# Kernel optimization log

Measured on AMD Instinct MI355X. Metric: run time of the kernel, lower is better.

The kernel has to match this reference:

```python
import jax, jax.numpy as jnp
import numpy as np

D_MODEL = 1024
N_HEADS = 16
HEAD_DIM = D_MODEL // N_HEADS
D_FF = 4 * D_MODEL


def _layernorm(x, g, b, eps=1e-5):
    mu = jnp.mean(x, axis=-1, keepdims=True)
    var = jnp.var(x, axis=-1, keepdims=True)
    return (x - mu) * jax.lax.rsqrt(var + eps) * g + b


def setup_inputs() -> dict:
    key = jax.random.key(0)
    ks = jax.random.split(key, 12)
    s = lambda fan_in: 1.0 / np.sqrt(fan_in)
    x = jax.random.normal(ks[0], (2, 2048, D_MODEL), dtype=jnp.float32)
    return {
        "x": x,
        "ln1_g": jnp.ones((D_MODEL,), jnp.float32),
        "ln1_b": jnp.zeros((D_MODEL,), jnp.float32),
        "w_qkv": jax.random.uniform(ks[1], (D_MODEL, 3 * D_MODEL), jnp.float32, -s(D_MODEL), s(D_MODEL)),
        "b_qkv": jax.random.uniform(ks[2], (3 * D_MODEL,), jnp.float32, -s(D_MODEL), s(D_MODEL)),
        "w_out": jax.random.uniform(ks[3], (D_MODEL, D_MODEL), jnp.float32, -s(D_MODEL), s(D_MODEL)),
        "b_out": jax.random.uniform(ks[4], (D_MODEL,), jnp.float32, -s(D_MODEL), s(D_MODEL)),
        "ln2_g": jnp.ones((D_MODEL,), jnp.float32),
        "ln2_b": jnp.zeros((D_MODEL,), jnp.float32),
        "w_ff1": jax.random.uniform(ks[5], (D_MODEL, D_FF), jnp.float32, -s(D_MODEL), s(D_MODEL)),
        "b_ff1": jax.random.uniform(ks[6], (D_FF,), jnp.float32, -s(D_MODEL), s(D_MODEL)),
        "w_ff2": jax.random.uniform(ks[7], (D_FF, D_MODEL), jnp.float32, -s(D_FF), s(D_FF)),
        "b_ff2": jax.random.uniform(ks[8], (D_MODEL,), jnp.float32, -s(D_FF), s(D_FF)),
    }


def reference(x, ln1_g, ln1_b, w_qkv, b_qkv, w_out, b_out,
              ln2_g, ln2_b, w_ff1, b_ff1, w_ff2, b_ff2):
    B, T, C = x.shape
    # --- pre-LN causal self-attention + residual ---
    h = _layernorm(x, ln1_g, ln1_b)
    qkv = h @ w_qkv + b_qkv                                  # [B,T,3C]
    qkv = qkv.reshape(B, T, 3, N_HEADS, HEAD_DIM)
    q, k, v = qkv[:, :, 0], qkv[:, :, 1], qkv[:, :, 2]       # [B,T,H,Dh]
    scores = jnp.einsum("bthd,bshd->bhts", q, k) / np.sqrt(HEAD_DIM).astype(np.float32)
    causal = jnp.tril(jnp.ones((T, T), dtype=bool))
    scores = jnp.where(causal, scores, -jnp.inf)
    weights = jax.nn.softmax(scores, axis=-1)                # [B,H,T,T]
    attn = jnp.einsum("bhts,bshd->bthd", weights, v).reshape(B, T, C)
    x = x + attn @ w_out + b_out
    # --- pre-LN GELU FFN + residual ---
    h = _layernorm(x, ln2_g, ln2_b)
    h = jax.nn.gelu(h @ w_ff1 + b_ff1, approximate=False)    # torch GELU = erf
    x = x + h @ w_ff2 + b_ff2
    return x
```

## Files before the change

kernel.cpp:

```cpp
#include <hip/hip_runtime.h>
#include <hip/hip_bf16.h>
#include <math.h>

#define TSEQ 2048
#define BATCH 2
#define CDIM 1024
#define NH 16
#define HD 64
#define DFF 4096
#define ROWS (BATCH*TSEQ)

typedef __attribute__((ext_vector_type(4))) float f32x4;
typedef __attribute__((ext_vector_type(8))) short bf16x8;
typedef __attribute__((ext_vector_type(4))) unsigned short u16x4;

__device__ __forceinline__ void gload_lds16(const void* g, void* l) {
    void* gv = const_cast<void*>(g);
    __builtin_amdgcn_global_load_lds((__attribute__((address_space(1))) void*)gv,
                                     (__attribute__((address_space(3))) void*)l, 16, 0, 0);
}

__device__ __forceinline__ unsigned short f2bf(float f) {
    unsigned int u = __float_as_uint(f);
    return (unsigned short)((u + 0x7FFFu + ((u >> 16) & 1u)) >> 16);
}
__device__ __forceinline__ float bf2f(unsigned short u) {
    return __uint_as_float((unsigned int)u << 16);
}
__device__ __forceinline__ unsigned int cvt_pk_bf16(float lo, float hi) {
    unsigned int r;
    asm("v_cvt_pk_bf16_f32 %0, %1, %2" : "=v"(r) : "v"(lo), "v"(hi));
    return r;
}
__device__ __forceinline__ float fast_gelu(float v) {
    float u = fmaf(0.044715f * v * v, v, v);
    float e = __expf(-1.5957691216057308f * u);
    return v * __builtin_amdgcn_rcpf(1.0f + e);
}

__global__ __launch_bounds__(256) void ln_kernel(const float* __restrict__ x,
                                                 const float* __restrict__ g,
                                                 const float* __restrict__ b,
                                                 unsigned short* __restrict__ out) {
    int row = blockIdx.x;
    int tid = threadIdx.x;
    const float* xr = x + (size_t)row * CDIM;
    float4 v = *(const float4*)(xr + tid * 4);
    float s  = v.x + v.y + v.z + v.w;
    float s2 = v.x*v.x + v.y*v.y + v.z*v.z + v.w*v.w;
    #pragma unroll
    for (int off = 32; off >= 1; off >>= 1) {
        s  += __shfl_down(s, off);
        s2 += __shfl_down(s2, off);
    }
    __shared__ float red[8];
    int wid = tid >> 6, lane = tid & 63;
    if (lane == 0) { red[wid] = s; red[wid + 4] = s2; }
    __syncthreads();
    float ts  = red[0] + red[1] + red[2] + red[3];
    float ts2 = red[4] + red[5] + red[6] + red[7];
    float mu  = ts * (1.0f / CDIM);
    float var = ts2 * (1.0f / CDIM) - mu * mu;
    float rstd = rsqrtf(var + 1e-5f);
    float4 gv = *(const float4*)(g + tid * 4);
    float4 bv = *(const float4*)(b + tid * 4);
    unsigned short o4[4];
    o4[0] = f2bf((v.x - mu) * rstd * gv.x + bv.x);
    o4[1] = f2bf((v.y - mu) * rstd * gv.y + bv.y);
    o4[2] = f2bf((v.z - mu) * rstd * gv.z + bv.z);
    o4[3] = f2bf((v.w - mu) * rstd * gv.w + bv.w);
    *(u16x4*)(out + (size_t)row * CDIM + tid * 4) = *(u16x4*)o4;
}

__global__ __launch_bounds__(256) void transpose_cast_kernel(const float* __restrict__ W,
                                                             unsigned short* __restrict__ Wt,
                                                             int K, int N) {
    __shared__ float T[64][65];
    int tid = threadIdx.x;
    int n0 = blockIdx.x * 64, k0 = blockIdx.y * 64;
    int kr = tid >> 4;
    int nc = (tid & 15) * 4;
    #pragma unroll
    for (int i = 0; i < 4; ++i) {
        float4 v = *(const float4*)&W[(size_t)(k0 + kr + i*16) * N + (n0 + nc)];
        T[kr + i*16][nc + 0] = v.x;
        T[kr + i*16][nc + 1] = v.y;
        T[kr + i*16][nc + 2] = v.z;
        T[kr + i*16][nc + 3] = v.w;
    }
    __syncthreads();
    int n  = tid >> 2;
    int kb = (tid & 3) * 16;
    unsigned short tmp[16];
    #pragma unroll
    for (int i = 0; i < 16; ++i) tmp[i] = f2bf(T[kb + i][n]);
    unsigned short* dst = Wt + (size_t)(n0 + n) * K + (k0 + kb);
    *(int4*)dst       = *(int4*)&tmp[0];
    *(int4*)(dst + 8) = *(int4*)&tmp[8];
}

__global__ __launch_bounds__(256) void kvfrag_kernel(const unsigned short* __restrict__ qkv,
                                                     unsigned short* __restrict__ kfrag,
                                                     unsigned short* __restrict__ vfrag) {
    __shared__ unsigned short Kt[64][72];
    __shared__ unsigned short Vt[64][72];
    const int tid = threadIdx.x;
    const int j  = blockIdx.x;
    const int bh = blockIdx.y;
    const int b = bh >> 4, h = bh & 15;
    {
        const int r  = tid >> 2;
        const int c0 = (tid & 3) * 16;
        const unsigned short* src = qkv + ((size_t)(b * TSEQ + j * 64 + r)) * 3072 + 1024 + h * 64 + c0;
        bf16x8 k0 = *(const bf16x8*)src;
        bf16x8 k1 = *(const bf16x8*)(src + 8);
        bf16x8 v0 = *(const bf16x8*)(src + 1024);
        bf16x8 v1 = *(const bf16x8*)(src + 1032);
        *(bf16x8*)&Kt[r][c0]     = k0;
        *(bf16x8*)&Kt[r][c0 + 8] = k1;
        *(bf16x8*)&Vt[r][c0]     = v0;
        *(bf16x8*)&Vt[r][c0 + 8] = v1;
    }
    __syncthreads();
    const int l  = tid & 63;
    const int qd = tid >> 6;
    const size_t tbase = ((size_t)(bh * 32 + j)) * 8 * 512;
    #pragma unroll
    for (int pass = 0; pass < 2; ++pass) {
        const int kc = qd + pass * 4;
        const int sb = kc >> 1, g = kc & 1;
        bf16x8 kv = *(const bf16x8*)&Kt[sb * 16 + (l & 15)][g * 32 + (l >> 4) * 8];
        *(bf16x8*)(kfrag + tbase + kc * 512 + l * 8) = kv;

        const int vc = qd + pass * 4;
        const int kb = vc >> 2, db = vc & 3;
        unsigned short tmp[8];
        #pragma unroll
        for (int i = 0; i < 8; ++i)
            tmp[i] = Vt[kb * 32 + (l >> 4) * 8 + i][db * 16 + (l & 15)];
        *(bf16x8*)(vfrag + tbase + vc * 512 + l * 8) = *(bf16x8*)tmp;
    }
}

template<int EPI>
__global__ __launch_bounds__(256) void gemm_kernel(const unsigned short* __restrict__ A,
                                                   const unsigned short* __restrict__ Bt,
                                                   const float* __restrict__ bias,
                                                   const float* __restrict__ res,
                                                   void* __restrict__ Cout,
                                                   int M, int N, int K, int nbx, int rpx) {
    __shared__ __align__(16) unsigned short As[128 * 64];
    __shared__ __align__(16) unsigned short Bs[128 * 64];
    const int tid = threadIdx.x;
    const int l   = tid & 63;
    const int w   = tid >> 6;
    const int wr  = (w >> 1) * 64;
    const int wc  = (w & 1) * 64;
    const int lin = blockIdx.x;
    const int xcd = lin & 7;
    const int idx = lin >> 3;
    const long brow = (long)(xcd * rpx + idx / nbx) * 128;
    const long bcol = (long)(idx % nbx) * 128;

    const int srow = tid >> 3;
    const int schk = ((tid & 7) ^ (srow & 7)) * 8;
    const unsigned short* gA = A  + (size_t)(brow + srow) * K + schk;
    const unsigned short* gB = Bt + (size_t)(bcol + srow) * K + schk;
    unsigned short* lA = As + tid * 8;
    unsigned short* lB = Bs + tid * 8;

    f32x4 acc[4][4];
    #pragma unroll
    for (int m = 0; m < 4; ++m)
        #pragma unroll
        for (int n = 0; n < 4; ++n) acc[m][n] = (f32x4){0.f, 0.f, 0.f, 0.f};

    for (int k0 = 0; k0 < K; k0 += 64) {
        #pragma unroll
        for (int p = 0; p < 4; ++p) {
            gload_lds16(gA + (size_t)(32 * p) * K + k0, lA + p * 2048);
            gload_lds16(gB + (size_t)(32 * p) * K + k0, lB + p * 2048);
        }
        __syncthreads();
        #pragma unroll
        for (int gg = 0; gg < 2; ++gg) {
            const int koff = ((gg * 4 + (l >> 4)) ^ (l & 7)) * 8;
            bf16x8 af[4], bf[4];
            #pragma unroll
            for (int m = 0; m < 4; ++m)
                af[m] = *(const bf16x8*)&As[(wr + m * 16 + (l & 15)) * 64 + koff];
            #pragma unroll
            for (int n = 0; n < 4; ++n)
                bf[n] = *(const bf16x8*)&Bs[(wc + n * 16 + (l & 15)) * 64 + koff];
            #pragma unroll
            for (int m = 0; m < 4; ++m)
                #pragma unroll
                for (int n = 0; n < 4; ++n)
                    acc[m][n] = __builtin_amdgcn_mfma_f32_16x16x32_bf16(af[m], bf[n], acc[m][n], 0, 0, 0);
        }
        __syncthreads();
    }

    #pragma unroll
    for (int m = 0; m < 4; ++m) {
        const int rown = wr + m * 16 + (l >> 4) * 4;
        #pragma unroll
        for (int n = 0; n < 4; ++n) {
            const long col = bcol + wc + n * 16 + (l & 15);
            const float bb = bias[col];
            #pragma unroll
            for (int r = 0; r < 4; ++r) {
                const long row = brow + rown + r;
                float v = acc[m][n][r] + bb;
                if (EPI == 1) {
                    v += res[row * N + col];
                    ((float*)Cout)[row * N + col] = v;
                } else if (EPI == 2) {
                    ((unsigned short*)Cout)[row * N + col] = f2bf(fast_gelu(v));
                } else {
                    ((unsigned short*)Cout)[row * N + col] = f2bf(v);
                }
            }
        }
    }
}

template<int EPI>
__global__ __launch_bounds__(256) void gemm64_kernel(const unsigned short* __restrict__ A,
                                                     const unsigned short* __restrict__ Bt,
                                                     const float* __restrict__ bias,
                                                     const float* __restrict__ res,
                                                     void* __restrict__ Cout,
                                                     int M, int N, int K, int nbx, int rpx) {
    __shared__ __align__(16) unsigned short As[3 * 64 * 64];
    __shared__ __align__(16) unsigned short Bs[3 * 128 * 64];
    const int tid = threadIdx.x;
    const int l   = tid & 63;
    const int w   = tid >> 6;
    const int wr  = (w >> 1) * 32;
    const int wc  = (w & 1) * 64;
    const int lin = blockIdx.x;
    const int xcd = lin & 7;
    const int idx = lin >> 3;
    const long brow = (long)(xcd * rpx + idx / nbx) * 64;
    const long bcol = (long)(idx % nbx) * 128;

    const int srow = tid >> 3;
    const int schk = ((tid & 7) ^ (srow & 7)) * 8;
    const unsigned short* gA = A  + (size_t)(brow + srow) * K + schk;
    const unsigned short* gB = Bt + (size_t)(bcol + srow) * K + schk;

    f32x4 acc[2][4];
    #pragma unroll
    for (int m = 0; m < 2; ++m)
        #pragma unroll
        for (int n = 0; n < 4; ++n) acc[m][n] = (f32x4){0.f, 0.f, 0.f, 0.f};

    #define STAGE64(buf, koff_)                                                        \
        do {                                                                           \
            unsigned short* lA_ = As + (buf) * 4096 + tid * 8;                         \
            unsigned short* lB_ = Bs + (buf) * 8192 + tid * 8;                         \
            _Pragma("unroll")                                                          \
            for (int p = 0; p < 2; ++p)                                                \
                gload_lds16(gA + (size_t)(32 * p) * K + (koff_), lA_ + p * 2048);      \
            _Pragma("unroll")                                                          \
            for (int p = 0; p < 4; ++p)                                                \
                gload_lds16(gB + (size_t)(32 * p) * K + (koff_), lB_ + p * 2048);      \
        } while (0)

    STAGE64(0, 0);
    STAGE64(1, 64);

    int cur = 0;
    for (int k0 = 0; k0 < K; k0 += 64) {
        if (k0 + 64 < K) asm volatile("s_waitcnt vmcnt(6)" ::: "memory");
        else             asm volatile("s_waitcnt vmcnt(0)" ::: "memory");
        __builtin_amdgcn_s_barrier();
        asm volatile("" ::: "memory");

        const unsigned short* cA = As + cur * 4096;
        const unsigned short* cB = Bs + cur * 8192;
        #pragma unroll
        for (int gg = 0; gg < 2; ++gg) {
            const int koff = ((gg * 4 + (l >> 4)) ^ (l & 7)) * 8;
            bf16x8 af[2], bf[4];
            #pragma unroll
            for (int m = 0; m < 2; ++m)
                af[m] = *(const bf16x8*)&cA[(wr + m * 16 + (l & 15)) * 64 + koff];
            #pragma unroll
            for (int n = 0; n < 4; ++n)
                bf[n] = *(const bf16x8*)&cB[(wc + n * 16 + (l & 15)) * 64 + koff];
            #pragma unroll
            for (int m = 0; m < 2; ++m)
                #pragma unroll
                for (int n = 0; n < 4; ++n)
                    acc[m][n] = __builtin_amdgcn_mfma_f32_16x16x32_bf16(af[m], bf[n], acc[m][n], 0, 0, 0);
        }

        if (k0 + 128 < K) {
            int nxt = cur + 2; if (nxt >= 3) nxt -= 3;
            STAGE64(nxt, k0 + 128);
        }
        cur = cur + 1; if (cur == 3) cur = 0;
    }
    #undef STAGE64

    #pragma unroll
    for (int m = 0; m < 2; ++m) {
        const int rown = wr + m * 16 + (l >> 4) * 4;
        #pragma unroll
        for (int n = 0; n < 4; ++n) {
            const long col = bcol + wc + n * 16 + (l & 15);
            const float bb = bias[col];
            #pragma unroll
            for (int r = 0; r < 4; ++r) {
                const long row = brow + rown + r;
                float v = acc[m][n][r] + bb;
                if (EPI == 1) {
                    v += res[row * N + col];
                    ((float*)Cout)[row * N + col] = v;
                } else if (EPI == 2) {
                    ((unsigned short*)Cout)[row * N + col] = f2bf(fast_gelu(v));
                } else {
                    ((unsigned short*)Cout)[row * N + col] = f2bf(v);
                }
            }
        }
    }
}

#define QSCALE 0.18033688011112042f
__global__ __launch_bounds__(64) void attn_kernel(const unsigned short* __restrict__ qkv,
                                                  const unsigned short* __restrict__ kfrag,
                                                  const unsigned short* __restrict__ vfrag,
                                                  unsigned short* __restrict__ out) {
    __shared__ __align__(16) unsigned short Ps[16 * 128];

    const int l    = threadIdx.x;
    const int q    = l & 15;
    const int g    = l >> 4;
    const int lin  = blockIdx.x;
    const int xcd  = lin & 7;
    const int rest = lin >> 3;
    const int h    = xcd + 8 * (rest & 1);
    const int b    = (rest >> 1) & 1;
    const int strip = 127 - (rest >> 2);
    const int jmax  = strip >> 2;
    const size_t rowbase = (size_t)b * TSEQ;
    const int bh = b * NH + h;
    const int qglob = strip * 16 + q;

    const unsigned short* kfb = kfrag + (size_t)bh * 32 * 8 * 512;
    const unsigned short* vfb = vfrag + (size_t)bh * 32 * 8 * 512;

    bf16x8 aq0, aq1;
    {
        const unsigned short* qp = qkv + (rowbase + qglob) * 3072 + h * 64 + g * 8;
        bf16x8 t0 = *(const bf16x8*)qp;
        bf16x8 t1 = *(const bf16x8*)(qp + 32);
        #pragma unroll
        for (int i = 0; i < 8; ++i) {
            aq0[i] = (short)f2bf(bf2f((unsigned short)t0[i]) * QSCALE);
            aq1[i] = (short)f2bf(bf2f((unsigned short)t1[i]) * QSCALE);
        }
    }

    float mrow = -INFINITY, lrow = 0.f;
    f32x4 o[4];
    #pragma unroll
    for (int d = 0; d < 4; ++d) o[d] = (f32x4){0.f, 0.f, 0.f, 0.f};

    for (int j = 0; j + 1 <= jmax; j += 2) {
        const bool diag2 = (j + 1 == jmax);

        bf16x8 kf[16];
        #pragma unroll
        for (int t = 0; t < 2; ++t)
            #pragma unroll
            for (int sb = 0; sb < 4; ++sb) {
                const unsigned short* kp = kfb + (size_t)((j + t) * 8 + sb * 2) * 512 + l * 8;
                kf[t * 8 + sb * 2]     = *(const bf16x8*)kp;
                kf[t * 8 + sb * 2 + 1] = *(const bf16x8*)(kp + 512);
            }

        f32x4 sf[8];
        __builtin_amdgcn_s_setprio(1);
        #pragma unroll
        for (int t = 0; t < 2; ++t)
            #pragma unroll
            for (int sb = 0; sb < 4; ++sb) {
                f32x4 acc = (f32x4){0.f, 0.f, 0.f, 0.f};
                acc = __builtin_amdgcn_mfma_f32_16x16x32_bf16(kf[t*8 + sb*2],     aq0, acc, 0, 0, 0);
                acc = __builtin_amdgcn_mfma_f32_16x16x32_bf16(kf[t*8 + sb*2 + 1], aq1, acc, 0, 0, 0);
                sf[t*4 + sb] = acc;
            }
        __builtin_amdgcn_s_setprio(0);

        bf16x8 vf[16];
        #pragma unroll
        for (int kb = 0; kb < 4; ++kb)
            #pragma unroll
            for (int db = 0; db < 4; ++db)
                vf[kb * 4 + db] = *(const bf16x8*)(vfb + (size_t)((j + (kb >> 1)) * 8 + (kb & 1) * 4 + db) * 512 + l * 8);

        if (diag2) {
            #pragma unroll
            for (int sb = 0; sb < 4; ++sb) {
                const int sg = (j + 1) * 64 + sb * 16 + 4 * g;
                #pragma unroll
                for (int r = 0; r < 4; ++r)
                    if (sg + r > qglob) sf[4 + sb][r] = -INFINITY;
            }
        }

        f32x4 mv = sf[0];
        #pragma unroll
        for (int i = 1; i < 8; ++i)
            #pragma unroll
            for (int r = 0; r < 4; ++r) mv[r] = fmaxf(mv[r], sf[i][r]);
        float mloc = fmaxf(fmaxf(mv[0], mv[1]), fmaxf(mv[2], mv[3]));
        mloc = fmaxf(mloc, __shfl_xor(mloc, 16));
        mloc = fmaxf(mloc, __shfl_xor(mloc, 32));
        const float mn = fmaxf(mrow, mloc);
        const float alpha = exp2f(mrow - mn);
        mrow = mn;

        float psum = 0.f;
        #pragma unroll
        for (int i = 0; i < 8; ++i) {
            const int t = i >> 2, sb = i & 3;
            float p0 = exp2f(sf[i][0] - mn);
            float p1 = exp2f(sf[i][1] - mn);
            float p2 = exp2f(sf[i][2] - mn);
            float p3 = exp2f(sf[i][3] - mn);
            psum += (p0 + p1) + (p2 + p3);
            unsigned int pk0 = cvt_pk_bf16(p0, p1);
            unsigned int pk1 = cvt_pk_bf16(p2, p3);
            const int c16 = (t * 8 + sb * 2 + (g >> 1)) ^ (q & 7);
            *(uint2*)((char*)Ps + q * 256 + c16 * 16 + (g & 1) * 8) = make_uint2(pk0, pk1);
        }
        psum += __shfl_xor(psum, 16);
        psum += __shfl_xor(psum, 32);
        lrow = lrow * alpha + psum;

        float al[4];
        #pragma unroll
        for (int r = 0; r < 4; ++r) al[r] = __shfl(alpha, g * 4 + r);
        #pragma unroll
        for (int d = 0; d < 4; ++d)
            #pragma unroll
            for (int r = 0; r < 4; ++r) o[d][r] *= al[r];

        __builtin_amdgcn_s_setprio(1);
        #pragma unroll
        for (int kb = 0; kb < 4; ++kb) {
            const int c16 = (kb * 4 + g) ^ (q & 7);
            bf16x8 pa = *(const bf16x8*)((const char*)Ps + q * 256 + c16 * 16);
            #pragma unroll
            for (int db = 0; db < 4; ++db)
                o[db] = __builtin_amdgcn_mfma_f32_16x16x32_bf16(pa, vf[kb * 4 + db], o[db], 0, 0, 0);
        }
        __builtin_amdgcn_s_setprio(0);
    }

    if ((jmax & 1) == 0) {
        const int j = jmax;
        bf16x8 kf[8];
        #pragma unroll
        for (int sb = 0; sb < 4; ++sb) {
            const unsigned short* kp = kfb + (size_t)(j * 8 + sb * 2) * 512 + l * 8;
            kf[sb * 2]     = *(const bf16x8*)kp;
            kf[sb * 2 + 1] = *(const bf16x8*)(kp + 512);
        }
        f32x4 sf[4];
        __builtin_amdgcn_s_setprio(1);
        #pragma unroll
        for (int sb = 0; sb < 4; ++sb) {
            f32x4 acc = (f32x4){0.f, 0.f, 0.f, 0.f};
            acc = __builtin_amdgcn_mfma_f32_16x16x32_bf16(kf[sb*2],     aq0, acc, 0, 0, 0);
            acc = __builtin_amdgcn_mfma_f32_16x16x32_bf16(kf[sb*2 + 1], aq1, acc, 0, 0, 0);
            sf[sb] = acc;
        }
        __builtin_amdgcn_s_setprio(0);

        bf16x8 vf[8];
        #pragma unroll
        for (int kb = 0; kb < 2; ++kb)
            #pragma unroll
            for (int db = 0; db < 4; ++db)
                vf[kb * 4 + db] = *(const bf16x8*)(vfb + (size_t)(j * 8 + kb * 4 + db) * 512 + l * 8);

        #pragma unroll
        for (int sb = 0; sb < 4; ++sb) {
            const int sg = j * 64 + sb * 16 + 4 * g;
            #pragma unroll
            for (int r = 0; r < 4; ++r)
                if (sg + r > qglob) sf[sb][r] = -INFINITY;
        }

        f32x4 mv = sf[0];
        #pragma unroll
        for (int i = 1; i < 4; ++i)
            #pragma unroll
            for (int r = 0; r < 4; ++r) mv[r] = fmaxf(mv[r], sf[i][r]);
        float mloc = fmaxf(fmaxf(mv[0], mv[1]), fmaxf(mv[2], mv[3]));
        mloc = fmaxf(mloc, __shfl_xor(mloc, 16));
        mloc = fmaxf(mloc, __shfl_xor(mloc, 32));
        const float mn = fmaxf(mrow, mloc);
        const float alpha = exp2f(mrow - mn);
        mrow = mn;

        float psum = 0.f;
        #pragma unroll
        for (int sb = 0; sb < 4; ++sb) {
            float p0 = exp2f(sf[sb][0] - mn);
            float p1 = exp2f(sf[sb][1] - mn);
            float p2 = exp2f(sf[sb][2] - mn);
            float p3 = exp2f(sf[sb][3] - mn);
            psum += (p0 + p1) + (p2 + p3);
            unsigned int pk0 = cvt_pk_bf16(p0, p1);
            unsigned int pk1 = cvt_pk_bf16(p2, p3);
            const int c16 = (sb * 2 + (g >> 1)) ^ (q & 7);
            *(uint2*)((char*)Ps + q * 256 + c16 * 16 + (g & 1) * 8) = make_uint2(pk0, pk1);
        }
        psum += __shfl_xor(psum, 16);
        psum += __shfl_xor(psum, 32);
        lrow = lrow * alpha + psum;

        float al[4];
        #pragma unroll
        for (int r = 0; r < 4; ++r) al[r] = __shfl(alpha, g * 4 + r);
        #pragma unroll
        for (int d = 0; d < 4; ++d)
            #pragma unroll
            for (int r = 0; r < 4; ++r) o[d][r] *= al[r];

        __builtin_amdgcn_s_setprio(1);
        #pragma unroll
        for (int kb = 0; kb < 2; ++kb) {
            const int c16 = (kb * 4 + g) ^ (q & 7);
            bf16x8 pa = *(const bf16x8*)((const char*)Ps + q * 256 + c16 * 16);
            #pragma unroll
            for (int db = 0; db < 4; ++db)
                o[db] = __builtin_amdgcn_mfma_f32_16x16x32_bf16(pa, vf[kb * 4 + db], o[db], 0, 0, 0);
        }
        __builtin_amdgcn_s_setprio(0);
    }

    float linv[4];
    #pragma unroll
    for (int r = 0; r < 4; ++r) linv[r] = 1.0f / __shfl(lrow, g * 4 + r);
    #pragma unroll
    for (int r = 0; r < 4; ++r) {
        const size_t rb = (rowbase + strip * 16 + g * 4 + r) * (size_t)CDIM + h * 64 + q;
        #pragma unroll
        for (int d = 0; d < 4; ++d)
            out[rb + d * 16] = f2bf(o[d][r] * linv[r]);
    }
}

extern "C" void kernel_launch(void* const* d_in, const int* in_sizes, int n_in,
                              void* d_out, int out_size, void* d_ws, size_t ws_size,
                              hipStream_t stream) {
    const float* x     = (const float*)d_in[0];
    const float* ln1_g = (const float*)d_in[1];
    const float* ln1_b = (const float*)d_in[2];
    const float* w_qkv = (const float*)d_in[3];
    const float* b_qkv = (const float*)d_in[4];
    const float* w_out = (const float*)d_in[5];
    const float* b_out = (const float*)d_in[6];
    const float* ln2_g = (const float*)d_in[7];
    const float* ln2_b = (const float*)d_in[8];
    const float* w_ff1 = (const float*)d_in[9];
    const float* b_ff1 = (const float*)d_in[10];
    const float* w_ff2 = (const float*)d_in[11];
    const float* b_ff2 = (const float*)d_in[12];
    float* out = (float*)d_out;

    char* wsb = (char*)d_ws;
    unsigned short* h_bf    = (unsigned short*)(wsb);
    unsigned short* qkv_bf  = (unsigned short*)(wsb + 8ll  * 1024 * 1024);
    unsigned short* attn_bf = (unsigned short*)(wsb + 32ll * 1024 * 1024);
    float*          x1      = (float*)         (wsb + 40ll * 1024 * 1024);
    unsigned short* kfrag   = (unsigned short*)(wsb + 40ll * 1024 * 1024);
    unsigned short* vfrag   = (unsigned short*)(wsb + 48ll * 1024 * 1024);
    unsigned short* wqkvT   = (unsigned short*)(wsb + 56ll * 1024 * 1024);
    unsigned short* woutT   = (unsigned short*)(wsb + 62ll * 1024 * 1024);
    unsigned short* wff1T   = (unsigned short*)(wsb + 64ll * 1024 * 1024);
    unsigned short* wff2T   = (unsigned short*)(wsb + 72ll * 1024 * 1024);
    unsigned short* ff1_bf  = (unsigned short*)(wsb + 8ll  * 1024 * 1024);

    transpose_cast_kernel<<<dim3(48, 16), 256, 0, stream>>>(w_qkv, wqkvT, 1024, 3072);
    transpose_cast_kernel<<<dim3(16, 16), 256, 0, stream>>>(w_out, woutT, 1024, 1024);
    transpose_cast_kernel<<<dim3(64, 16), 256, 0, stream>>>(w_ff1, wff1T, 1024, 4096);
    transpose_cast_kernel<<<dim3(16, 64), 256, 0, stream>>>(w_ff2, wff2T, 4096, 1024);

    ln_kernel<<<ROWS, 256, 0, stream>>>(x, ln1_g, ln1_b, h_bf);
    gemm_kernel<0><<<768, 256, 0, stream>>>(h_bf, wqkvT, b_qkv, nullptr, qkv_bf, ROWS, 3072, 1024, 24, 4);
    kvfrag_kernel<<<dim3(32, 32), 256, 0, stream>>>(qkv_bf, kfrag, vfrag);
    attn_kernel<<<4096, 64, 0, stream>>>(qkv_bf, kfrag, vfrag, attn_bf);
    gemm64_kernel<1><<<512, 256, 0, stream>>>(attn_bf, woutT, b_out, x, x1, ROWS, 1024, 1024, 8, 8);
    ln_kernel<<<ROWS, 256, 0, stream>>>(x1, ln2_g, ln2_b, h_bf);
    gemm_kernel<2><<<1024, 256, 0, stream>>>(h_bf, wff1T, b_ff1, nullptr, ff1_bf, ROWS, 4096, 1024, 32, 4);
    gemm64_kernel<1><<<512, 256, 0, stream>>>(ff1_bf, wff2T, b_ff2, x1, (float*)out, ROWS, 1024, 4096, 8, 8);
}
```

Baseline: 254.5 us.

## Triple-buffer GEMM LDS tiles with K=32 steps and async prefetch

Restructures the GEMM main loop into a three-stage LDS ring buffer with 32-wide K slices. Global-to-LDS loads for slice k+2 are issued while slice k is computed, using vmcnt waits and a single barrier per iteration instead of two syncthreads. The aim is to hide global load latency behind MFMA work. In exchange it adds more iterations and barriers per K step, and the overwrite safety of the ring buffer depends on that single barrier placement.

```diff
diff --git a/kernel.cpp b/kernel.cpp
--- a/kernel.cpp
+++ b/kernel.cpp
@@ -149,8 +149,8 @@
                                                    const float* __restrict__ res,
                                                    void* __restrict__ Cout,
                                                    int M, int N, int K, int nbx, int rpx) {
-    __shared__ __align__(16) unsigned short As[128 * 64];
-    __shared__ __align__(16) unsigned short Bs[128 * 64];
+    __shared__ __align__(16) unsigned short As[3 * 4096];
+    __shared__ __align__(16) unsigned short Bs[3 * 4096];
     const int tid = threadIdx.x;
     const int l   = tid & 63;
     const int w   = tid >> 6;
@@ -162,12 +162,10 @@
     const long brow = (long)(xcd * rpx + idx / nbx) * 128;
     const long bcol = (long)(idx % nbx) * 128;
 
-    const int srow = tid >> 3;
-    const int schk = ((tid & 7) ^ (srow & 7)) * 8;
+    const int srow = tid >> 2;
+    const int schk = ((tid & 3) ^ (srow & 3)) * 8;
     const unsigned short* gA = A  + (size_t)(brow + srow) * K + schk;
     const unsigned short* gB = Bt + (size_t)(bcol + srow) * K + schk;
-    unsigned short* lA = As + tid * 8;
-    unsigned short* lB = Bs + tid * 8;
 
     f32x4 acc[4][4];
     #pragma unroll
@@ -175,31 +173,49 @@
         #pragma unroll
         for (int n = 0; n < 4; ++n) acc[m][n] = (f32x4){0.f, 0.f, 0.f, 0.f};
 
-    for (int k0 = 0; k0 < K; k0 += 64) {
-        #pragma unroll
-        for (int p = 0; p < 4; ++p) {
-            gload_lds16(gA + (size_t)(32 * p) * K + k0, lA + p * 2048);
-            gload_lds16(gB + (size_t)(32 * p) * K + k0, lB + p * 2048);
-        }
-        __syncthreads();
-        #pragma unroll
-        for (int gg = 0; gg < 2; ++gg) {
-            const int koff = ((gg * 4 + (l >> 4)) ^ (l & 7)) * 8;
-            bf16x8 af[4], bf[4];
-            #pragma unroll
-            for (int m = 0; m < 4; ++m)
-                af[m] = *(const bf16x8*)&As[(wr + m * 16 + (l & 15)) * 64 + koff];
+    #define STAGE128(buf, koff_)                                                       \
+        do {                                                                           \
+            unsigned short* lA_ = As + (buf) * 4096 + tid * 8;                         \
+            unsigned short* lB_ = Bs + (buf) * 4096 + tid * 8;                         \
+            gload_lds16(gA + (koff_), lA_);                                            \
+            gload_lds16(gA + (size_t)64 * K + (koff_), lA_ + 2048);                    \
+            gload_lds16(gB + (koff_), lB_);                                            \
+            gload_lds16(gB + (size_t)64 * K + (koff_), lB_ + 2048);                    \
+        } while (0)
+
+    STAGE128(0, 0);
+    STAGE128(1, 32);
+
+    int cur = 0;
+    for (int k0 = 0; k0 < K; k0 += 32) {
+        if (k0 + 32 < K) asm volatile("s_waitcnt vmcnt(4)" ::: "memory");
+        else             asm volatile("s_waitcnt vmcnt(0)" ::: "memory");
+        __builtin_amdgcn_s_barrier();
+        asm volatile("" ::: "memory");
+
+        const unsigned short* cA = As + cur * 4096 + (wr >> 6) * 2048;
+        const unsigned short* cB = Bs + cur * 4096 + (wc >> 6) * 2048;
+        const int koff = ((l >> 4) ^ (l & 3)) * 8;
+        bf16x8 af[4], bf[4];
+        #pragma unroll
+        for (int m = 0; m < 4; ++m)
+            af[m] = *(const bf16x8*)&cA[(m * 16 + (l & 15)) * 32 + koff];
+        #pragma unroll
+        for (int n = 0; n < 4; ++n)
+            bf[n] = *(const bf16x8*)&cB[(n * 16 + (l & 15)) * 32 + koff];
+        #pragma unroll
+        for (int m = 0; m < 4; ++m)
             #pragma unroll
             for (int n = 0; n < 4; ++n)
-                bf[n] = *(const bf16x8*)&Bs[(wc + n * 16 + (l & 15)) * 64 + koff];
-            #pragma unroll
-            for (int m = 0; m < 4; ++m)
-                #pragma unroll
-                for (int n = 0; n < 4; ++n)
-                    acc[m][n] = __builtin_amdgcn_mfma_f32_16x16x32_bf16(af[m], bf[n], acc[m][n], 0, 0, 0);
-        }
-        __syncthreads();
-    }
+                acc[m][n] = __builtin_amdgcn_mfma_f32_16x16x32_bf16(af[m], bf[n], acc[m][n], 0, 0, 0);
+
+        if (k0 + 64 < K) {
+            int nxt = cur + 2; if (nxt >= 3) nxt -= 3;
+            STAGE128(nxt, k0 + 64);
+        }
+        cur = cur + 1; if (cur == 3) cur = 0;
+    }
+    #undef STAGE128
 
     #pragma unroll
     for (int m = 0; m < 4; ++m) {
```

Result: faster. 242.1 us (-4.9%).
